# Optimization experiments

Measured on AMD Instinct MI355X. Metric: run time of the kernel, lower is better.

Reference implementation:

```python
import jax, jax.numpy as jnp
import numpy as np

N = 50000   # nodes
E = 800000  # edges
IN, H, O, C = 128, 256, 256, 64
G = 64      # graphs in batch


def setup_inputs() -> dict:
    key = jax.random.key(0)
    ks = jax.random.split(key, 10)
    x = jax.random.normal(ks[0], (N, IN), dtype=jnp.float32)
    edge_index = jax.random.randint(ks[1], (2, E), 0, N, dtype=jnp.int32)
    batch = jnp.sort(jax.random.randint(ks[2], (N,), 0, G, dtype=jnp.int32))
    # learned params (PyG GCNConv: weight [in, out] + bias [out]; nn.Linear)
    W1 = jax.random.normal(ks[3], (IN, H), dtype=jnp.float32) / np.sqrt(IN)
    b1 = jnp.zeros((H,), dtype=jnp.float32)
    W2 = jax.random.normal(ks[4], (H, O), dtype=jnp.float32) / np.sqrt(H)
    b2 = jnp.zeros((O,), dtype=jnp.float32)
    Wfc = jax.random.normal(ks[5], (O, C), dtype=jnp.float32) / np.sqrt(O)
    bfc = jnp.zeros((C,), dtype=jnp.float32)
    return {"x": x, "edge_index": edge_index, "batch": batch,
            "W1": W1, "b1": b1, "W2": W2, "b2": b2, "Wfc": Wfc, "bfc": bfc}


def reference(x, edge_index, batch, W1, b1, W2, b2, Wfc, bfc):
    src, dst = edge_index[0], edge_index[1]
    # degree with self-loops (PyG GCNConv default: add_self_loops=True, sym norm)
    deg = jax.ops.segment_sum(jnp.ones((E,), x.dtype), dst, num_segments=N) + 1.0
    dinv = jax.lax.rsqrt(deg)                      # D^{-1/2}
    edge_norm = (dinv[src] * dinv[dst])[:, None]   # [E, 1]
    self_norm = (dinv * dinv)[:, None]             # [N, 1] self-loop weight

    def gcn_conv(h, W, b):
        h = h @ W                                  # transform first (PyG order)
        agg = jax.ops.segment_sum(h[src] * edge_norm, dst, num_segments=N)
        return agg + h * self_norm + b

    h = jax.nn.gelu(gcn_conv(x, W1, b1), approximate=False)  # nn.GELU exact
    h = gcn_conv(h, W2, b2)

    # global_mean_pool over graph ids
    cnt = jax.ops.segment_sum(jnp.ones((N,), h.dtype), batch, num_segments=G)
    pooled = jax.ops.segment_sum(h, batch, num_segments=G) / jnp.maximum(cnt, 1.0)[:, None]
    return pooled @ Wfc + bfc                      # [G, C]
```

## Files before the change

kernel.cpp:

```cpp
#include <hip/hip_runtime.h>
#include <hip/hip_bf16.h>
#include <hip/hip_fp16.h>
#include <math.h>

#define NNODES 50000
#define NEDGES 800000
#define FIN 128
#define FH 256
#define NG 64
#define NC 64
#define NP 50176
#define SPLITX_ITEMS (NNODES * FIN / 4)
#define SPLITX_BLOCKS ((SPLITX_ITEMS + 255) / 256)
#define W1T_BLOCKS (FIN * 256 / 256)
#define GEMM_MB ((NNODES + 127) / 128)
#define GEMM_BLKS (GEMM_MB * 2)
#define QTR (NP / 4)

#define NBUCK 196
#define BCAP 5120
#define BIN_CHUNK 2048
#define BIN_BLOCKS ((NEDGES + BIN_CHUNK - 1) / BIN_CHUNK)
#define K1_BLOCKS (BIN_BLOCKS + SPLITX_BLOCKS + W1T_BLOCKS)

typedef unsigned short bhalf;
typedef __attribute__((ext_vector_type(8))) short bf16x8;
typedef __attribute__((ext_vector_type(4))) float f32x4;
typedef __attribute__((ext_vector_type(4))) unsigned short u16x4;

__device__ inline bhalf f2bf_rn(float f) {
    unsigned int u = __float_as_uint(f);
    u += 0x7FFFu + ((u >> 16) & 1u);
    return (bhalf)(u >> 16);
}
__device__ inline float bf2f(bhalf h) { return __uint_as_float(((unsigned int)h) << 16); }
__device__ inline float2 bfpair(unsigned int u) {
    return make_float2(__uint_as_float(u << 16), __uint_as_float(u & 0xFFFF0000u));
}


__global__ __launch_bounds__(256)
void k1_kernel(const int* __restrict__ src, const int* __restrict__ dst,
               int* __restrict__ bcur, unsigned int* __restrict__ binned,
               const float* __restrict__ x, bhalf* __restrict__ xb,
               const float* __restrict__ W1, bhalf* __restrict__ w1t) {
    if (blockIdx.x >= BIN_BLOCKS) {
        int b = blockIdx.x - BIN_BLOCKS;
        if (b < SPLITX_BLOCKS) {
            int i = b * 256 + threadIdx.x;
            if (i < SPLITX_ITEMS) {
                float4 v = *reinterpret_cast<const float4*>(&x[i * 4]);
                u16x4 o = {f2bf_rn(v.x), f2bf_rn(v.y), f2bf_rn(v.z), f2bf_rn(v.w)};
                *reinterpret_cast<u16x4*>(&xb[i * 4]) = o;
            }
        } else {
            int i = (b - SPLITX_BLOCKS) * 256 + threadIdx.x;
            int k = i >> 8, n = i & 255;
            w1t[n * FIN + k] = f2bf_rn(W1[i]);
        }
        return;
    }
    __shared__ int hist[NBUCK];
    __shared__ int base[NBUCK];
    __shared__ int gb[NBUCK];
    __shared__ int lcur[NBUCK];
    __shared__ int scan_tmp[256];
    __shared__ unsigned int stage[BIN_CHUNK];
    __shared__ unsigned char bid[BIN_CHUNK];
    int t = threadIdx.x;
    int e0 = blockIdx.x * BIN_CHUNK;
    for (int i = t; i < NBUCK; i += 256) hist[i] = 0;
    __syncthreads();
#pragma unroll
    for (int k = 0; k < BIN_CHUNK / 256; k++) {
        int e = e0 + k * 256 + t;
        if (e < NEDGES) atomicAdd(&hist[dst[e] >> 8], 1);
    }
    __syncthreads();
    int v = (t < NBUCK) ? hist[t] : 0;
    scan_tmp[t] = v;
    __syncthreads();
#pragma unroll
    for (int off = 1; off < 256; off <<= 1) {
        int xx = (t >= off) ? scan_tmp[t - off] : 0;
        __syncthreads();
        scan_tmp[t] += xx;
        __syncthreads();
    }
    if (t < NBUCK) {
        int ex = scan_tmp[t] - v;
        base[t] = ex;
        lcur[t] = ex;
        gb[t] = (v > 0) ? atomicAdd(&bcur[t], v) : 0;
    }
    __syncthreads();
#pragma unroll
    for (int k = 0; k < BIN_CHUNK / 256; k++) {
        int e = e0 + k * 256 + t;
        if (e < NEDGES) {
            int s = src[e], d = dst[e];
            int b = d >> 8;
            int lp = atomicAdd(&lcur[b], 1);
            stage[lp] = (unsigned int)s | ((unsigned int)(d & 255) << 16);
            bid[lp] = (unsigned char)b;
        }
    }
    __syncthreads();
    int total = base[NBUCK - 1] + hist[NBUCK - 1];
    for (int i = t; i < total; i += 256) {
        int b = bid[i];
        binned[(size_t)b * BCAP + gb[b] + (i - base[b])] = stage[i];
    }
}


__global__ __launch_bounds__(256)
void place_kernel(const unsigned int* __restrict__ binned, const int* __restrict__ bcur,
                  int* __restrict__ row_start, float* __restrict__ dinv,
                  unsigned int* __restrict__ edata) {
    __shared__ unsigned int stage[BCAP];
    __shared__ int sc[256];
    __shared__ int deg[256];
    __shared__ int lex[256];
    __shared__ int lcur[256];
    __shared__ unsigned short dih[256];
    __shared__ int s_ebase, s_cnt;
    int b = blockIdx.x, t = threadIdx.x;
    int c = (t < NBUCK) ? bcur[t] : 0;
    sc[t] = c;
    __syncthreads();
#pragma unroll
    for (int off = 1; off < 256; off <<= 1) {
        int x = (t >= off) ? sc[t - off] : 0;
        __syncthreads();
        sc[t] += x;
        __syncthreads();
    }
    if (t == b) { s_ebase = sc[t] - c; s_cnt = c; }
    deg[t] = 0;
    __syncthreads();
    int cnt = s_cnt, eb = s_ebase;
    const unsigned int* bp = &binned[(size_t)b * BCAP];
    for (int i = t; i < cnt; i += 256) stage[i] = bp[i];
    __syncthreads();
    for (int i = t; i < cnt; i += 256) atomicAdd(&deg[(stage[i] >> 16) & 255], 1);
    __syncthreads();
    int d = deg[t];
    float di = rsqrtf((float)d + 1.0f);
    int gn = (b << 8) + t;
    if (gn < NNODES) dinv[gn] = di;
    dih[t] = __half_as_ushort(__float2half(di));
    sc[t] = d;
    __syncthreads();
#pragma unroll
    for (int off = 1; off < 256; off <<= 1) {
        int x = (t >= off) ? sc[t - off] : 0;
        __syncthreads();
        sc[t] += x;
        __syncthreads();
    }
    int lexv = sc[t] - d;
    lex[t] = lexv;
    lcur[t] = 0;
    if (gn <= NNODES) row_start[gn] = eb + lexv;
    __syncthreads();
    for (int i = t; i < cnt; i += 256) {
        unsigned int e = stage[i];
        int dl = (e >> 16) & 255;
        int pos = eb + lex[dl] + atomicAdd(&lcur[dl], 1);
        edata[pos] = (e & 0xFFFFu) | ((unsigned int)dih[dl] << 16);
    }
}


__global__ __launch_bounds__(256)
void gather128_kernel(const bhalf* __restrict__ xb, const unsigned int* __restrict__ edata,
                      const int* __restrict__ row_start, const float* __restrict__ dinv,
                      bhalf* __restrict__ z, int Nn) {
    int node = blockIdx.x * 4 + (threadIdx.x >> 6);
    if (node >= Nn) return;
    int lane = threadIdx.x & 63;
    int st = row_start[node];
    int cnt = row_start[node + 1] - st;
    float ax = 0.0f, ay = 0.0f;
    int j = 0;
    for (; j + 3 < cnt; j += 4) {
        unsigned int e0 = edata[st + j],     e1 = edata[st + j + 1];
        unsigned int e2 = edata[st + j + 2], e3 = edata[st + j + 3];
        int s0 = e0 & 0xFFFFu, s1 = e1 & 0xFFFFu, s2 = e2 & 0xFFFFu, s3 = e3 & 0xFFFFu;
        float2 v0 = bfpair(*reinterpret_cast<const unsigned int*>(&xb[(size_t)s0 * FIN + lane * 2]));
        float2 v1 = bfpair(*reinterpret_cast<const unsigned int*>(&xb[(size_t)s1 * FIN + lane * 2]));
        float2 v2 = bfpair(*reinterpret_cast<const unsigned int*>(&xb[(size_t)s2 * FIN + lane * 2]));
        float2 v3 = bfpair(*reinterpret_cast<const unsigned int*>(&xb[(size_t)s3 * FIN + lane * 2]));
        float n0 = dinv[s0], n1 = dinv[s1], n2 = dinv[s2], n3 = dinv[s3];
        ax += v0.x * n0 + v1.x * n1 + v2.x * n2 + v3.x * n3;
        ay += v0.y * n0 + v1.y * n1 + v2.y * n2 + v3.y * n3;
    }
    for (; j < cnt; j++) {
        unsigned int e0 = edata[st + j];
        int s0 = e0 & 0xFFFFu;
        float2 v0 = bfpair(*reinterpret_cast<const unsigned int*>(&xb[(size_t)s0 * FIN + lane * 2]));
        float n0 = dinv[s0];
        ax += v0.x * n0; ay += v0.y * n0;
    }
    float dn = dinv[node];
    float2 xv = bfpair(*reinterpret_cast<const unsigned int*>(&xb[(size_t)node * FIN + lane * 2]));
    ushort2 o = {f2bf_rn(dn * (ax + xv.x * dn)), f2bf_rn(dn * (ay + xv.y * dn))};
    *reinterpret_cast<ushort2*>(&z[(size_t)node * FIN + lane * 2]) = o;
}


__global__ __launch_bounds__(256)
void wt_build_kernel(const unsigned int* __restrict__ edata, const int* __restrict__ row_start,
                     const int* __restrict__ batch, const float* __restrict__ dinv,
                     bhalf* __restrict__ wthi, bhalf* __restrict__ wtlo) {
    __shared__ float acc[QTR];
    int g = blockIdx.x >> 2;
    int q = blockIdx.x & 3;
    int base = q * QTR;
    for (int i = threadIdx.x; i < QTR; i += 256) acc[i] = 0.0f;
    int lo = 0, hi = NNODES;
    while (lo < hi) { int m = (lo + hi) >> 1; if (batch[m] < g) lo = m + 1; else hi = m; }
    int na = lo;
    hi = NNODES;
    while (lo < hi) { int m = (lo + hi) >> 1; if (batch[m] < g + 1) lo = m + 1; else hi = m; }
    int nb = lo;
    int pa = row_start[na];
    int pb = row_start[nb];
    __syncthreads();
    for (int p = pa + threadIdx.x; p < pb; p += 256) {
        unsigned int e = edata[p];
        int s = (int)(e & 0xFFFFu) - base;
        if ((unsigned int)s < (unsigned int)QTR)
            atomicAdd(&acc[s], __half2float(__ushort_as_half((unsigned short)(e >> 16))));
    }
    __syncthreads();
    size_t rowo = (size_t)g * NP + base;
    for (int i = threadIdx.x; i < QTR; i += 256) {
        int s = base + i;
        float dv = (s < NNODES) ? dinv[s] : 0.0f;
        float v = acc[i];
        if (s >= na && s < nb) v += dv;
        v *= dv;
        bhalf hb = f2bf_rn(v);
        wthi[rowo + i] = hb;
        wtlo[rowo + i] = f2bf_rn(v - bf2f(hb));
    }
}


__global__ __launch_bounds__(256)
void gemmq_kernel(const bhalf* __restrict__ A, const bhalf* __restrict__ Bt,
                  const float* __restrict__ bias, const bhalf* __restrict__ wthi,
                  const bhalf* __restrict__ wtlo, float* __restrict__ qpart, int M) {
    __shared__ alignas(16) bhalf smem[2 * 128 * 72];
    bhalf* As = smem;
    bhalf* Bs = smem + 128 * 72;
    const int tid  = threadIdx.x;
    const int lane = tid & 63;
    const int wave = tid >> 6;
    const int quad = lane >> 4;
    const int l15  = lane & 15;
    const int wm = (wave & 1) * 64;
    const int wn = (wave >> 1) * 64;
    const int bm = (blockIdx.x >> 1) * 128;
    const int bn = (blockIdx.x & 1) * 128;

    f32x4 acc[4][4] = {};

    for (int k0 = 0; k0 < FIN; k0 += 64) {
#pragma unroll
        for (int i = 0; i < 4; i++) {
            int chunk = tid + i * 256;
            int r = chunk >> 3, c16 = chunk & 7;
            int gm = bm + r;
            float4 va = make_float4(0.f, 0.f, 0.f, 0.f);
            if (gm < M) va = *reinterpret_cast<const float4*>(&A[(size_t)gm * FIN + k0 + c16 * 8]);
            *reinterpret_cast<float4*>(&As[r * 72 + c16 * 8]) = va;
            float4 vb = *reinterpret_cast<const float4*>(&Bt[(size_t)(bn + r) * FIN + k0 + c16 * 8]);
            *reinterpret_cast<float4*>(&Bs[r * 72 + c16 * 8]) = vb;
        }
        __syncthreads();
#pragma unroll
        for (int kk = 0; kk < 64; kk += 32) {
            bf16x8 af[4], bfr[4];
#pragma unroll
            for (int mi = 0; mi < 4; mi++)
                af[mi] = *reinterpret_cast<const bf16x8*>(&As[(wm + mi * 16 + l15) * 72 + kk + quad * 8]);
#pragma unroll
            for (int ni = 0; ni < 4; ni++)
                bfr[ni] = *reinterpret_cast<const bf16x8*>(&Bs[(wn + ni * 16 + l15) * 72 + kk + quad * 8]);
#pragma unroll
            for (int mi = 0; mi < 4; mi++)
#pragma unroll
                for (int ni = 0; ni < 4; ni++)
                    acc[mi][ni] = __builtin_amdgcn_mfma_f32_16x16x32_bf16(af[mi], bfr[ni], acc[mi][ni], 0, 0, 0);
        }
        __syncthreads();
    }

    bhalf* h1s = smem;
#pragma unroll
    for (int mi = 0; mi < 4; mi++) {
        int node0 = wm + mi * 16 + quad * 4;
#pragma unroll
        for (int ni = 0; ni < 4; ni++) {
            int col = wn + ni * 16 + l15;
            float bv = bias[bn + col];
            u16x4 o;
#pragma unroll
            for (int r = 0; r < 4; r++) {
                float v = acc[mi][ni][r] + bv;
                v = 0.5f * v * (1.0f + erff(v * 0.70710678118654752f));
                o[r] = f2bf_rn(v);
            }
            *reinterpret_cast<u16x4*>(&h1s[col * 136 + node0]) = o;
        }
    }
    __syncthreads();

    f32x4 qacc[4][2] = {};
    const int c0 = wave * 32;
#pragma unroll
    for (int kk2 = 0; kk2 < 128; kk2 += 32) {
        bf16x8 bfr[2];
#pragma unroll
        for (int ct = 0; ct < 2; ct++)
            bfr[ct] = *reinterpret_cast<const bf16x8*>(&h1s[(c0 + ct * 16 + l15) * 136 + kk2 + quad * 8]);
        size_t nodeg = (size_t)(bm + kk2 + quad * 8);
#pragma unroll
        for (int gt = 0; gt < 4; gt++) {
            bf16x8 afh = *reinterpret_cast<const bf16x8*>(&wthi[(size_t)(gt * 16 + l15) * NP + nodeg]);
            bf16x8 afl = *reinterpret_cast<const bf16x8*>(&wtlo[(size_t)(gt * 16 + l15) * NP + nodeg]);
#pragma unroll
            for (int ct = 0; ct < 2; ct++) {
                qacc[gt][ct] = __builtin_amdgcn_mfma_f32_16x16x32_bf16(afh, bfr[ct], qacc[gt][ct], 0, 0, 0);
                qacc[gt][ct] = __builtin_amdgcn_mfma_f32_16x16x32_bf16(afl, bfr[ct], qacc[gt][ct], 0, 0, 0);
            }
        }
    }
    float* qp = &qpart[(size_t)blockIdx.x * NG * 128];
#pragma unroll
    for (int gt = 0; gt < 4; gt++) {
#pragma unroll
        for (int ct = 0; ct < 2; ct++) {
            int col = c0 + ct * 16 + l15;
#pragma unroll
            for (int r = 0; r < 4; r++)
                qp[(gt * 16 + quad * 4 + r) * 128 + col] = qacc[gt][ct][r];
        }
    }
}


__global__ __launch_bounds__(256)
void p2fc_kernel(const float* __restrict__ qpart, const float* __restrict__ W2,
                 const float* __restrict__ b2, const int* __restrict__ batch,
                 const float* __restrict__ Wfc, const float* __restrict__ bfc,
                 float* __restrict__ out) {
    __shared__ float qg[FH];
    __shared__ float ps[FH];
    int g = blockIdx.x;
    int t = threadIdx.x;
    int half = t >> 7, kc = t & 127;
    float s = 0.0f;
    for (int m = 0; m < GEMM_MB; m++)
        s += qpart[(size_t)(m * 2 + half) * NG * 128 + (size_t)g * 128 + kc];
    qg[half * 128 + kc] = s;
    int lo = 0, hi = NNODES;
    while (lo < hi) { int m = (lo + hi) >> 1; if (batch[m] < g) lo = m + 1; else hi = m; }
    int a = lo;
    lo = 0; hi = NNODES;
    while (lo < hi) { int m = (lo + hi) >> 1; if (batch[m] < g + 1) lo = m + 1; else hi = m; }
    float inv = 1.0f / fmaxf((float)(lo - a), 1.0f);
    __syncthreads();
    float acc = 0.0f;
    for (int k = 0; k < FH; k++)
        acc += qg[k] * W2[k * FH + t];
    ps[t] = acc * inv + b2[t];
    __syncthreads();
    if (t < NC) {
        float a2 = 0.0f;
        for (int cc = 0; cc < FH; cc++)
            a2 += ps[cc] * Wfc[cc * NC + t];
        out[g * NC + t] = a2 + bfc[t];
    }
}


extern "C" void kernel_launch(void* const* d_in, const int* in_sizes, int n_in,
                              void* d_out, int out_size, void* d_ws, size_t ws_size,
                              hipStream_t stream) {
    const float* x    = (const float*)d_in[0];
    const int*   ei   = (const int*)d_in[1];
    const int*   batch= (const int*)d_in[2];
    const float* W1   = (const float*)d_in[3];
    const float* b1   = (const float*)d_in[4];
    const float* W2   = (const float*)d_in[5];
    const float* b2   = (const float*)d_in[6];
    const float* Wfc  = (const float*)d_in[7];
    const float* bfc  = (const float*)d_in[8];
    float* out = (float*)d_out;

    const int* src = ei;
    const int* dst = ei + NEDGES;

    bhalf* xb        = (bhalf*)d_ws;
    bhalf* zb        = xb + (size_t)NNODES * FIN;
    unsigned int* edata  = (unsigned int*)(zb + (size_t)NNODES * FIN);
    unsigned int* binned = edata + NEDGES;
    int*   row_start = (int*)(binned + (size_t)NBUCK * BCAP);
    int*   bcur      = row_start + NNODES + 256;
    float* dinv      = (float*)(bcur + 256);
    bhalf* w1t       = (bhalf*)(dinv + NNODES + 256);
    bhalf* wthi      = w1t + 256 * FIN;
    bhalf* wtlo      = wthi + (size_t)NG * NP;
    float* qpart     = (float*)(wtlo + (size_t)NG * NP);

    (void)hipMemsetAsync(bcur, 0, NBUCK * 4, stream);

    k1_kernel<<<K1_BLOCKS, 256, 0, stream>>>(src, dst, bcur, binned, x, xb, W1, w1t);
    place_kernel<<<NBUCK, 256, 0, stream>>>(binned, bcur, row_start, dinv, edata);

    gather128_kernel<<<(NNODES + 3) / 4, 256, 0, stream>>>(xb, edata, row_start, dinv,
                                                           zb, NNODES);
    wt_build_kernel<<<NG * 4, 256, 0, stream>>>(edata, row_start, batch, dinv, wthi, wtlo);

    gemmq_kernel<<<GEMM_BLKS, 256, 0, stream>>>(zb, w1t, b1, wthi, wtlo, qpart, NNODES);

    p2fc_kernel<<<NG, FH, 0, stream>>>(qpart, W2, b2, batch, Wfc, bfc, out);
}
```

Before: 247.9 us.

## Use single fp16 pooling weights, preload them, and split qpart reduction

Replaces the bf16 hi/lo split of the pooling weight matrix with a single fp16 copy. The second GEMM stage now does half as many MFMAs and reads half as much weight data, and those weights are loaded into registers at kernel start so the load overlaps the first GEMM. The GELU output is also stored as fp16. A separate qreduce kernel parallelises the partial-sum reduction over blocks that p2fc used to do serially per graph. The cost is reduced precision from fp16 range and mantissa limits, plus higher register pressure from the preloaded weights.

```diff
diff --git a/kernel.cpp b/kernel.cpp
--- a/kernel.cpp
+++ b/kernel.cpp
@@ -25,6 +25,7 @@
 
 typedef unsigned short bhalf;
 typedef __attribute__((ext_vector_type(8))) short bf16x8;
+typedef __attribute__((ext_vector_type(8))) _Float16 f16x8;
 typedef __attribute__((ext_vector_type(4))) float f32x4;
 typedef __attribute__((ext_vector_type(4))) unsigned short u16x4;
 
@@ -33,7 +34,6 @@
     u += 0x7FFFu + ((u >> 16) & 1u);
     return (bhalf)(u >> 16);
 }
-__device__ inline float bf2f(bhalf h) { return __uint_as_float(((unsigned int)h) << 16); }
 __device__ inline float2 bfpair(unsigned int u) {
     return make_float2(__uint_as_float(u << 16), __uint_as_float(u & 0xFFFF0000u));
 }
@@ -213,7 +213,7 @@
 __global__ __launch_bounds__(256)
 void wt_build_kernel(const unsigned int* __restrict__ edata, const int* __restrict__ row_start,
                      const int* __restrict__ batch, const float* __restrict__ dinv,
-                     bhalf* __restrict__ wthi, bhalf* __restrict__ wtlo) {
+                     unsigned short* __restrict__ wt16) {
     __shared__ float acc[QTR];
     int g = blockIdx.x >> 2;
     int q = blockIdx.x & 3;
@@ -242,17 +242,15 @@
         float v = acc[i];
         if (s >= na && s < nb) v += dv;
         v *= dv;
-        bhalf hb = f2bf_rn(v);
-        wthi[rowo + i] = hb;
-        wtlo[rowo + i] = f2bf_rn(v - bf2f(hb));
+        wt16[rowo + i] = __half_as_ushort(__float2half(v));
     }
 }
 
 
 __global__ __launch_bounds__(256)
 void gemmq_kernel(const bhalf* __restrict__ A, const bhalf* __restrict__ Bt,
-                  const float* __restrict__ bias, const bhalf* __restrict__ wthi,
-                  const bhalf* __restrict__ wtlo, float* __restrict__ qpart, int M) {
+                  const float* __restrict__ bias, const unsigned short* __restrict__ wt16,
+                  float* __restrict__ qpart, int M) {
     __shared__ alignas(16) bhalf smem[2 * 128 * 72];
     bhalf* As = smem;
     bhalf* Bs = smem + 128 * 72;
@@ -266,6 +264,14 @@
     const int bm = (blockIdx.x >> 1) * 128;
     const int bn = (blockIdx.x & 1) * 128;
 
+    f16x8 wreg[4][4];
+#pragma unroll
+    for (int ki = 0; ki < 4; ki++)
+#pragma unroll
+        for (int gt = 0; gt < 4; gt++)
+            wreg[ki][gt] = *reinterpret_cast<const f16x8*>(
+                &wt16[(size_t)(gt * 16 + l15) * NP + bm + ki * 32 + quad * 8]);
+
     f32x4 acc[4][4] = {};
 
     for (int k0 = 0; k0 < FIN; k0 += 64) {
@@ -312,7 +318,7 @@
             for (int r = 0; r < 4; r++) {
                 float v = acc[mi][ni][r] + bv;
                 v = 0.5f * v * (1.0f + erff(v * 0.70710678118654752f));
-                o[r] = f2bf_rn(v);
+                o[r] = __half_as_ushort(__float2half(v));
             }
             *reinterpret_cast<u16x4*>(&h1s[col * 136 + node0]) = o;
         }
@@ -322,22 +328,16 @@
     f32x4 qacc[4][2] = {};
     const int c0 = wave * 32;
 #pragma unroll
-    for (int kk2 = 0; kk2 < 128; kk2 += 32) {
-        bf16x8 bfr[2];
+    for (int ki = 0; ki < 4; ki++) {
+        f16x8 bfr[2];
 #pragma unroll
         for (int ct = 0; ct < 2; ct++)
-            bfr[ct] = *reinterpret_cast<const bf16x8*>(&h1s[(c0 + ct * 16 + l15) * 136 + kk2 + quad * 8]);
-        size_t nodeg = (size_t)(bm + kk2 + quad * 8);
-#pragma unroll
-        for (int gt = 0; gt < 4; gt++) {
-            bf16x8 afh = *reinterpret_cast<const bf16x8*>(&wthi[(size_t)(gt * 16 + l15) * NP + nodeg]);
-            bf16x8 afl = *reinterpret_cast<const bf16x8*>(&wtlo[(size_t)(gt * 16 + l15) * NP + nodeg]);
-#pragma unroll
-            for (int ct = 0; ct < 2; ct++) {
-                qacc[gt][ct] = __builtin_amdgcn_mfma_f32_16x16x32_bf16(afh, bfr[ct], qacc[gt][ct], 0, 0, 0);
-                qacc[gt][ct] = __builtin_amdgcn_mfma_f32_16x16x32_bf16(afl, bfr[ct], qacc[gt][ct], 0, 0, 0);
-            }
-        }
+            bfr[ct] = *reinterpret_cast<const f16x8*>(&h1s[(c0 + ct * 16 + l15) * 136 + ki * 32 + quad * 8]);
+#pragma unroll
+        for (int gt = 0; gt < 4; gt++)
+#pragma unroll
+            for (int ct = 0; ct < 2; ct++)
+                qacc[gt][ct] = __builtin_amdgcn_mfma_f32_16x16x32_f16(wreg[ki][gt], bfr[ct], qacc[gt][ct], 0, 0, 0);
     }
     float* qp = &qpart[(size_t)blockIdx.x * NG * 128];
 #pragma unroll
@@ -354,19 +354,36 @@
 
 
 __global__ __launch_bounds__(256)
-void p2fc_kernel(const float* __restrict__ qpart, const float* __restrict__ W2,
+void qreduce_kernel(const float* __restrict__ qpart, float* __restrict__ qg) {
+    __shared__ float red[256];
+    int g = blockIdx.x >> 2;
+    int chunk = blockIdx.x & 3;
+    int half = chunk >> 1;
+    int col128 = (chunk & 1) * 64 + (threadIdx.x & 63);
+    int mi = threadIdx.x >> 6;
+    float s = 0.0f;
+    for (int m = mi; m < GEMM_MB; m += 4)
+        s += qpart[(size_t)(m * 2 + half) * NG * 128 + (size_t)g * 128 + col128];
+    red[threadIdx.x] = s;
+    __syncthreads();
+    if (mi == 0) {
+        int kc = threadIdx.x;
+        qg[(size_t)g * FH + half * 128 + col128] =
+            red[kc] + red[64 + kc] + red[128 + kc] + red[192 + kc];
+    }
+}
+
+
+__global__ __launch_bounds__(256)
+void p2fc_kernel(const float* __restrict__ qg, const float* __restrict__ W2,
                  const float* __restrict__ b2, const int* __restrict__ batch,
                  const float* __restrict__ Wfc, const float* __restrict__ bfc,
                  float* __restrict__ out) {
-    __shared__ float qg[FH];
+    __shared__ float qgl[FH];
     __shared__ float ps[FH];
     int g = blockIdx.x;
     int t = threadIdx.x;
-    int half = t >> 7, kc = t & 127;
-    float s = 0.0f;
-    for (int m = 0; m < GEMM_MB; m++)
-        s += qpart[(size_t)(m * 2 + half) * NG * 128 + (size_t)g * 128 + kc];
-    qg[half * 128 + kc] = s;
+    qgl[t] = qg[(size_t)g * FH + t];
     int lo = 0, hi = NNODES;
     while (lo < hi) { int m = (lo + hi) >> 1; if (batch[m] < g) lo = m + 1; else hi = m; }
     int a = lo;
@@ -376,7 +393,7 @@
     __syncthreads();
     float acc = 0.0f;
     for (int k = 0; k < FH; k++)
-        acc += qg[k] * W2[k * FH + t];
+        acc += qgl[k] * W2[k * FH + t];
     ps[t] = acc * inv + b2[t];
     __syncthreads();
     if (t < NC) {
@@ -413,9 +430,9 @@
     int*   bcur      = row_start + NNODES + 256;
     float* dinv      = (float*)(bcur + 256);
     bhalf* w1t       = (bhalf*)(dinv + NNODES + 256);
-    bhalf* wthi      = w1t + 256 * FIN;
-    bhalf* wtlo      = wthi + (size_t)NG * NP;
-    float* qpart     = (float*)(wtlo + (size_t)NG * NP);
+    unsigned short* wt16 = (unsigned short*)(w1t + 256 * FIN);
+    float* qg        = (float*)(wt16 + (size_t)NG * NP);
+    float* qpart     = qg + (size_t)NG * FH;
 
     (void)hipMemsetAsync(bcur, 0, NBUCK * 4, stream);
 
@@ -424,9 +441,10 @@
 
     gather128_kernel<<<(NNODES + 3) / 4, 256, 0, stream>>>(xb, edata, row_start, dinv,
                                                            zb, NNODES);
-    wt_build_kernel<<<NG * 4, 256, 0, stream>>>(edata, row_start, batch, dinv, wthi, wtlo);
-
-    gemmq_kernel<<<GEMM_BLKS, 256, 0, stream>>>(zb, w1t, b1, wthi, wtlo, qpart, NNODES);
-
-    p2fc_kernel<<<NG, FH, 0, stream>>>(qpart, W2, b2, batch, Wfc, bfc, out);
-}
+    wt_build_kernel<<<NG * 4, 256, 0, stream>>>(edata, row_start, batch, dinv, wt16);
+
+    gemmq_kernel<<<GEMM_BLKS, 256, 0, stream>>>(zb, w1t, b1, wt16, qpart, NNODES);
+
+    qreduce_kernel<<<NG * 4, 256, 0, stream>>>(qpart, qg);
+    p2fc_kernel<<<NG, FH, 0, stream>>>(qg, W2, b2, batch, Wfc, bfc, out);
+}
```

Result: no change. 251.1 us (+1.3%).
